# Kernel optimization log

Hardware: AMD Instinct MI355X
Metric: run time of the kernel (lower is better)

Reference implementation:

```python
import jax, jax.numpy as jnp
import numpy as np

N, E, D, R = 50000, 800000, 256, 16


def setup_inputs() -> dict:
    key = jax.random.key(0)
    ks = jax.random.split(key, 6)
    x = jax.random.normal(ks[0], (N, D), dtype=jnp.float32)
    edge_index = jax.random.randint(ks[1], (2, E), 0, N)
    edge_type = jax.random.randint(ks[2], (E,), 0, R)
    # FastRGCNConv params (num_bases=None): full relation weight, root weight, bias
    weight = jax.random.normal(ks[3], (R, D, 1), dtype=jnp.float32) / np.float32(np.sqrt(D))
    root = jax.random.normal(ks[4], (D, 1), dtype=jnp.float32) / np.float32(np.sqrt(D))
    bias = jnp.zeros((1,), dtype=jnp.float32)
    return dict(x=x, edge_index=edge_index, edge_type=edge_type,
                weight=weight, root=root, bias=bias)


def reference(x, edge_index, edge_type, weight, root, bias):
    n = x.shape[0]
    src, dst = edge_index[0], edge_index[1]  # messages flow src (j) -> dst (i)
    # per-edge relation-wise transform: (x_j @ W[r])  with out_channels == 1
    w_e = weight[edge_type, :, 0]                   # [E, D] gather of relation weights
    msg = jnp.sum(x[src] * w_e, axis=-1)            # [E] per-edge scalar message
    # mean aggregation over incoming edges (scatter-add / degree)
    agg = jax.ops.segment_sum(msg, dst, num_segments=n)                   # [N]
    cnt = jax.ops.segment_sum(jnp.ones_like(msg), dst, num_segments=n)    # [N]
    mean = agg / jnp.maximum(cnt, 1.0)
    # root transform + bias, then tanh nonlinearity (min_score is None)
    score = jnp.tanh(mean + (x @ root)[:, 0] + bias[0])                   # [N]
    x_out = x * score[:, None]
    return x_out, score
```

## Files before the change

### kernel.cpp

```cpp
#include <hip/hip_runtime.h>
#include <math.h>

#define D 256
#define NREL 16
#define CHUNK 6250
#define BPC 32
#define LDST 129

typedef float f4v __attribute__((ext_vector_type(4)));

__global__ __launch_bounds__(256) void rgcn_y_kernel(
    const float* __restrict__ x, const float* __restrict__ w,
    const float* __restrict__ root, float* __restrict__ y,
    float* __restrict__ xr, int n)
{
    __shared__ float lds[64 * LDST];
    const int t = threadIdx.x;
    const int nl = t & 63;
    const int rg = __builtin_amdgcn_readfirstlane(t >> 6);
    const int node = blockIdx.x * 64 + nl;
    const int base = blockIdx.x * 64;

    const float* w0 = w + (size_t)(rg * 4 + 0) * D;
    const float* w1 = w + (size_t)(rg * 4 + 1) * D;
    const float* w2 = w + (size_t)(rg * 4 + 2) * D;
    const float* w3 = w + (size_t)(rg * 4 + 3) * D;
    const float* w4 = (rg == 3) ? root : w0;

    float acc0 = 0.f, acc1 = 0.f, acc2 = 0.f, acc3 = 0.f, accR = 0.f;

    #pragma unroll
    for (int h = 0; h < 2; ++h) {
        #pragma unroll
        for (int k = 0; k < 8; ++k) {
            int flat = k * 256 + t;
            int snl  = flat >> 5;
            int f4i  = flat & 31;
            int gn   = base + snl;
            float4 v = make_float4(0.f, 0.f, 0.f, 0.f);
            if (gn < n)
                v = *reinterpret_cast<const float4*>(
                        x + (size_t)gn * D + h * 128 + f4i * 4);
            int a = snl * LDST + f4i * 4;
            lds[a + 0] = v.x; lds[a + 1] = v.y;
            lds[a + 2] = v.z; lds[a + 3] = v.w;
        }
        __syncthreads();

        const float* h0 = w0 + h * 128;
        const float* h1 = w1 + h * 128;
        const float* h2 = w2 + h * 128;
        const float* h3 = w3 + h * 128;
        const float* h4 = w4 + h * 128;
        #pragma unroll 16
        for (int d = 0; d < 128; ++d) {
            float xv = lds[nl * LDST + d];
            acc0 = fmaf(xv, h0[d], acc0);
            acc1 = fmaf(xv, h1[d], acc1);
            acc2 = fmaf(xv, h2[d], acc2);
            acc3 = fmaf(xv, h3[d], acc3);
            accR = fmaf(xv, h4[d], accR);
        }
        if (h == 0) __syncthreads();
    }

    if (node < n) {
        float4 o; o.x = acc0; o.y = acc1; o.z = acc2; o.w = acc3;
        *reinterpret_cast<float4*>(y + (size_t)node * NREL + rg * 4) = o;
        if (rg == 3) xr[node] = accR;
    }
}

__global__ __launch_bounds__(1024) void rgcn_edge_scan_kernel(
    const int* __restrict__ src, const int* __restrict__ dst,
    const int* __restrict__ et, const float* __restrict__ y,
    float2* __restrict__ partial, int e, int sl)
{
    __shared__ float lsum[CHUNK];
    __shared__ float lcnt[CHUNK];
    const int t = threadIdx.x;
    const int c = blockIdx.x / BPC;
    const int b = blockIdx.x % BPC;
    const int base = c * CHUNK;

    for (int j = t; j < CHUNK; j += 1024) { lsum[j] = 0.f; lcnt[j] = 0.f; }
    __syncthreads();

    const int slice0 = b * sl;
    const int rem = e - slice0;
    if (rem > 0) {
        const int gmax = (min(sl, rem) + 3) >> 2;
        for (int g = t; g < gmax; g += 1024) {
            int idx = slice0 + g * 4;
            if (idx + 3 < e) {
                int4 d4 = *reinterpret_cast<const int4*>(dst + idx);
                int4 s4 = *reinterpret_cast<const int4*>(src + idx);
                int4 r4 = *reinterpret_cast<const int4*>(et + idx);
                int loc0 = d4.x - base, loc1 = d4.y - base;
                int loc2 = d4.z - base, loc3 = d4.w - base;
                if ((unsigned)loc0 < (unsigned)CHUNK) {
                    atomicAdd(&lsum[loc0], y[(size_t)s4.x * NREL + r4.x]);
                    atomicAdd(&lcnt[loc0], 1.0f);
                }
                if ((unsigned)loc1 < (unsigned)CHUNK) {
                    atomicAdd(&lsum[loc1], y[(size_t)s4.y * NREL + r4.y]);
                    atomicAdd(&lcnt[loc1], 1.0f);
                }
                if ((unsigned)loc2 < (unsigned)CHUNK) {
                    atomicAdd(&lsum[loc2], y[(size_t)s4.z * NREL + r4.z]);
                    atomicAdd(&lcnt[loc2], 1.0f);
                }
                if ((unsigned)loc3 < (unsigned)CHUNK) {
                    atomicAdd(&lsum[loc3], y[(size_t)s4.w * NREL + r4.w]);
                    atomicAdd(&lcnt[loc3], 1.0f);
                }
            } else {
                for (int k = idx; k < e; ++k) {
                    int loc = dst[k] - base;
                    if ((unsigned)loc < (unsigned)CHUNK) {
                        atomicAdd(&lsum[loc], y[(size_t)src[k] * NREL + et[k]]);
                        atomicAdd(&lcnt[loc], 1.0f);
                    }
                }
            }
        }
    }
    __syncthreads();

    float2* p = partial + ((size_t)(c * BPC + b)) * CHUNK;
    for (int j = t; j < CHUNK; j += 1024)
        p[j] = make_float2(lsum[j], lcnt[j]);
}

__global__ __launch_bounds__(256) void rgcn_finish_kernel(
    const float2* __restrict__ partial, const float* __restrict__ xr,
    const float* __restrict__ bias, const float* __restrict__ x,
    float* __restrict__ out_x, float* __restrict__ out_score, int n)
{
    __shared__ float ssum[32], scnt[32], sc[32];
    const int t = threadIdx.x;
    const int base = blockIdx.x * 32;

    if (t < 32) { ssum[t] = 0.f; scnt[t] = 0.f; }
    __syncthreads();

    {
        int nl = t & 31;
        int bg = t >> 5;
        int node = base + nl;
        float s = 0.f, cN = 0.f;
        if (node < n) {
            int c = node / CHUNK;
            int j = node - c * CHUNK;
            const float2* p = partial + (size_t)c * BPC * CHUNK + j;
            #pragma unroll
            for (int b = 0; b < 4; ++b) {
                float2 v = p[(size_t)(bg * 4 + b) * CHUNK];
                s += v.x; cN += v.y;
            }
        }
        atomicAdd(&ssum[nl], s);
        atomicAdd(&scnt[nl], cN);
    }
    __syncthreads();

    if (t < 32) {
        int node = base + t;
        if (node < n) {
            float m = ssum[t] / fmaxf(scnt[t], 1.0f);
            float v = tanhf(m + xr[node] + bias[0]);
            sc[t] = v;
            out_score[node] = v;
        }
    }
    __syncthreads();

    #pragma unroll
    for (int k = 0; k < 8; ++k) {
        int nl = k * 4 + (t >> 6);
        int f4 = t & 63;
        int node = base + nl;
        if (node < n) {
            float s = sc[nl];
            float4 v = *reinterpret_cast<const float4*>(
                           x + (size_t)node * D + f4 * 4);
            v.x *= s; v.y *= s; v.z *= s; v.w *= s;
            f4v vo = {v.x, v.y, v.z, v.w};
            __builtin_nontemporal_store(
                vo, (f4v*)(out_x + (size_t)node * D + f4 * 4));
        }
    }
}

__global__ __launch_bounds__(256) void rgcn_reduce_score_kernel(
    const float2* __restrict__ partial, const float* __restrict__ xr,
    const float* __restrict__ bias, float* __restrict__ score, int n)
{
    int i = blockIdx.x * 256 + threadIdx.x;
    if (i < n) {
        int c = i / CHUNK;
        int j = i - c * CHUNK;
        const float2* p = partial + (size_t)c * BPC * CHUNK + j;
        float s = 0.f, cN = 0.f;
        #pragma unroll 8
        for (int b = 0; b < BPC; ++b) {
            float2 v = p[(size_t)b * CHUNK];
            s += v.x; cN += v.y;
        }
        float m = s / fmaxf(cN, 1.0f);
        score[i] = tanhf(m + xr[i] + bias[0]);
    }
}

__global__ __launch_bounds__(256) void rgcn_scale_kernel(
    const float* __restrict__ x, const float* __restrict__ score,
    float* __restrict__ xo, int n)
{
    int gid = blockIdx.x * 256 + threadIdx.x;
    int node = gid >> 6;
    int f4 = gid & 63;
    if (node < n) {
        float s = score[node];
        float4 v = *reinterpret_cast<const float4*>(
                       x + (size_t)node * D + f4 * 4);
        v.x *= s; v.y *= s; v.z *= s; v.w *= s;
        *reinterpret_cast<float4*>(xo + (size_t)node * D + f4 * 4) = v;
    }
}

extern "C" void kernel_launch(void* const* d_in, const int* in_sizes, int n_in,
                              void* d_out, int out_size, void* d_ws, size_t ws_size,
                              hipStream_t stream)
{
    const float* x    = (const float*)d_in[0];
    const int*   ei   = (const int*)d_in[1];
    const int*   et   = (const int*)d_in[2];
    const float* w    = (const float*)d_in[3];
    const float* root = (const float*)d_in[4];
    const float* bias = (const float*)d_in[5];

    const int n = in_sizes[0] / D;
    const int e = in_sizes[2];

    float* out       = (float*)d_out;
    float* out_x     = out;
    float* out_score = out + (size_t)n * D;

    const int C = (n + CHUNK - 1) / CHUNK;
    const int sl = ((((e + BPC - 1) / BPC) + 3) & ~3);

    const size_t part_f = (size_t)C * BPC * CHUNK * 2;
    const size_t need_f = part_f + (size_t)n * (NREL + 1);
    const bool use_ws = (ws_size >= need_f * sizeof(float));

    float* sb;
    if (use_ws)
        sb = (float*)d_ws;
    else {
        size_t ts = (((size_t)n * D - need_f) & ~(size_t)1);
        sb = out_x + ts;
    }
    float2* partial = (float2*)sb;
    float*  y  = sb + part_f;
    float*  xr = y + (size_t)n * NREL;

    dim3 blk(256);
    rgcn_y_kernel<<<dim3((n + 63) / 64), blk, 0, stream>>>(x, w, root, y, xr, n);

    rgcn_edge_scan_kernel<<<dim3(C * BPC), dim3(1024), 0, stream>>>(
        ei, ei + e, et, y, partial, e, sl);

    if (use_ws) {
        rgcn_finish_kernel<<<dim3((n + 31) / 32), blk, 0, stream>>>(
            partial, xr, bias, x, out_x, out_score, n);
    } else {
        rgcn_reduce_score_kernel<<<dim3((n + 255) / 256), blk, 0, stream>>>(
            partial, xr, bias, out_score, n);
        rgcn_scale_kernel<<<dim3((int)(((size_t)n * 64 + 255) / 256)), blk, 0, stream>>>(
            x, out_score, out_x, n);
    }
}
```

Measured before the change: 61.22 us.

## Rewrite node-relation projection to use direct coalesced loads and shuffle reduction

The projection kernel no longer stages x tiles through LDS with barriers. Each 16-lane group now reads two node rows straight from global memory with float4 loads, computes partial dot products against all 16 relation weights and the root vector, and reduces them with xor shuffles. It then writes one relation output per lane. This removes the LDS round trip and the syncthreads, but costs many more registers per thread (34 accumulators) and adds shuffle reduction work.

```diff
diff --git a/kernel.cpp b/kernel.cpp
--- a/kernel.cpp
+++ b/kernel.cpp
@@ -5,7 +5,6 @@
 #define NREL 16
 #define CHUNK 6250
 #define BPC 32
-#define LDST 129
 
 typedef float f4v __attribute__((ext_vector_type(4)));
 
@@ -14,60 +13,76 @@
     const float* __restrict__ root, float* __restrict__ y,
     float* __restrict__ xr, int n)
 {
-    __shared__ float lds[64 * LDST];
-    const int t = threadIdx.x;
-    const int nl = t & 63;
-    const int rg = __builtin_amdgcn_readfirstlane(t >> 6);
-    const int node = blockIdx.x * 64 + nl;
-    const int base = blockIdx.x * 64;
-
-    const float* w0 = w + (size_t)(rg * 4 + 0) * D;
-    const float* w1 = w + (size_t)(rg * 4 + 1) * D;
-    const float* w2 = w + (size_t)(rg * 4 + 2) * D;
-    const float* w3 = w + (size_t)(rg * 4 + 3) * D;
-    const float* w4 = (rg == 3) ? root : w0;
-
-    float acc0 = 0.f, acc1 = 0.f, acc2 = 0.f, acc3 = 0.f, accR = 0.f;
-
-    #pragma unroll
-    for (int h = 0; h < 2; ++h) {
+    const int t    = threadIdx.x;
+    const int lane = t & 63;
+    const int wv   = t >> 6;
+    const int grp  = lane >> 4;
+    const int s    = lane & 15;
+    const int node0 = blockIdx.x * 32 + wv * 8 + grp;
+    const int node1 = node0 + 4;
+
+    float accA[NREL + 1], accB[NREL + 1];
+    #pragma unroll
+    for (int r = 0; r <= NREL; ++r) { accA[r] = 0.f; accB[r] = 0.f; }
+
+    const bool okA = (node0 < n);
+    const bool okB = (node1 < n);
+    const float* xrowA = x + (size_t)node0 * D;
+    const float* xrowB = x + (size_t)node1 * D;
+
+    #pragma unroll
+    for (int k = 0; k < 4; ++k) {
+        const int off = k * 64 + s * 4;
+        float4 xa = make_float4(0.f, 0.f, 0.f, 0.f);
+        float4 xb = make_float4(0.f, 0.f, 0.f, 0.f);
+        if (okA) xa = *reinterpret_cast<const float4*>(xrowA + off);
+        if (okB) xb = *reinterpret_cast<const float4*>(xrowB + off);
         #pragma unroll
-        for (int k = 0; k < 8; ++k) {
-            int flat = k * 256 + t;
-            int snl  = flat >> 5;
-            int f4i  = flat & 31;
-            int gn   = base + snl;
-            float4 v = make_float4(0.f, 0.f, 0.f, 0.f);
-            if (gn < n)
-                v = *reinterpret_cast<const float4*>(
-                        x + (size_t)gn * D + h * 128 + f4i * 4);
-            int a = snl * LDST + f4i * 4;
-            lds[a + 0] = v.x; lds[a + 1] = v.y;
-            lds[a + 2] = v.z; lds[a + 3] = v.w;
-        }
-        __syncthreads();
-
-        const float* h0 = w0 + h * 128;
-        const float* h1 = w1 + h * 128;
-        const float* h2 = w2 + h * 128;
-        const float* h3 = w3 + h * 128;
-        const float* h4 = w4 + h * 128;
-        #pragma unroll 16
-        for (int d = 0; d < 128; ++d) {
-            float xv = lds[nl * LDST + d];
-            acc0 = fmaf(xv, h0[d], acc0);
-            acc1 = fmaf(xv, h1[d], acc1);
-            acc2 = fmaf(xv, h2[d], acc2);
-            acc3 = fmaf(xv, h3[d], acc3);
-            accR = fmaf(xv, h4[d], accR);
-        }
-        if (h == 0) __syncthreads();
-    }
-
-    if (node < n) {
-        float4 o; o.x = acc0; o.y = acc1; o.z = acc2; o.w = acc3;
-        *reinterpret_cast<float4*>(y + (size_t)node * NREL + rg * 4) = o;
-        if (rg == 3) xr[node] = accR;
+        for (int r = 0; r < NREL; ++r) {
+            float4 wv4 = *reinterpret_cast<const float4*>(
+                             w + (size_t)r * D + off);
+            accA[r] = fmaf(xa.x, wv4.x, accA[r]);
+            accA[r] = fmaf(xa.y, wv4.y, accA[r]);
+            accA[r] = fmaf(xa.z, wv4.z, accA[r]);
+            accA[r] = fmaf(xa.w, wv4.w, accA[r]);
+            accB[r] = fmaf(xb.x, wv4.x, accB[r]);
+            accB[r] = fmaf(xb.y, wv4.y, accB[r]);
+            accB[r] = fmaf(xb.z, wv4.z, accB[r]);
+            accB[r] = fmaf(xb.w, wv4.w, accB[r]);
+        }
+        float4 rv = *reinterpret_cast<const float4*>(root + off);
+        accA[NREL] = fmaf(xa.x, rv.x, accA[NREL]);
+        accA[NREL] = fmaf(xa.y, rv.y, accA[NREL]);
+        accA[NREL] = fmaf(xa.z, rv.z, accA[NREL]);
+        accA[NREL] = fmaf(xa.w, rv.w, accA[NREL]);
+        accB[NREL] = fmaf(xb.x, rv.x, accB[NREL]);
+        accB[NREL] = fmaf(xb.y, rv.y, accB[NREL]);
+        accB[NREL] = fmaf(xb.z, rv.z, accB[NREL]);
+        accB[NREL] = fmaf(xb.w, rv.w, accB[NREL]);
+    }
+
+    #pragma unroll
+    for (int r = 0; r <= NREL; ++r) {
+        #pragma unroll
+        for (int m = 8; m >= 1; m >>= 1) {
+            accA[r] += __shfl_xor(accA[r], m, 16);
+            accB[r] += __shfl_xor(accB[r], m, 16);
+        }
+    }
+
+    float ya = accA[0], yb = accB[0];
+    #pragma unroll
+    for (int r = 1; r < NREL; ++r) {
+        if (s == r) { ya = accA[r]; yb = accB[r]; }
+    }
+
+    if (okA) {
+        y[(size_t)node0 * NREL + s] = ya;
+        if (s == 0) xr[node0] = accA[NREL];
+    }
+    if (okB) {
+        y[(size_t)node1 * NREL + s] = yb;
+        if (s == 0) xr[node1] = accB[NREL];
     }
 }
 
@@ -265,7 +280,7 @@
     float*  xr = y + (size_t)n * NREL;
 
     dim3 blk(256);
-    rgcn_y_kernel<<<dim3((n + 63) / 64), blk, 0, stream>>>(x, w, root, y, xr, n);
+    rgcn_y_kernel<<<dim3((n + 31) / 32), blk, 0, stream>>>(x, w, root, y, xr, n);
 
     rgcn_edge_scan_kernel<<<dim3(C * BPC), dim3(1024), 0, stream>>>(
         ei, ei + e, et, y, partial, e, sl);
```

Result: slower. 64.52 us (+5.4%).

## Restructure y kernel to 512 threads with transposed swizzled LDS tile

Applied to the files above, without the earlier changes.

The per-node relation projection kernel now loads the whole 64x256 x tile into LDS in one pass, stored transposed with a rotation swizzle to avoid bank conflicts, instead of two padded half-tiles. Each block runs 8 waves that each compute 2 relations (the last wave also computes the root projection), replacing 4 waves of 4 relations. This doubles the waves available for latency hiding and halves the per-thread FMA chain, at the cost of 64 KB of LDS per block, which limits occupancy, and an uneven extra load on the last wave.

```diff
diff --git a/kernel.cpp b/kernel.cpp
--- a/kernel.cpp
+++ b/kernel.cpp
@@ -5,69 +5,72 @@
 #define NREL 16
 #define CHUNK 6250
 #define BPC 32
-#define LDST 129
 
 typedef float f4v __attribute__((ext_vector_type(4)));
 
-__global__ __launch_bounds__(256) void rgcn_y_kernel(
+__global__ __launch_bounds__(512) void rgcn_y_kernel(
     const float* __restrict__ x, const float* __restrict__ w,
     const float* __restrict__ root, float* __restrict__ y,
     float* __restrict__ xr, int n)
 {
-    __shared__ float lds[64 * LDST];
-    const int t = threadIdx.x;
-    const int nl = t & 63;
-    const int rg = __builtin_amdgcn_readfirstlane(t >> 6);
-    const int node = blockIdx.x * 64 + nl;
+    __shared__ float lds[D * 64];
+    const int t    = threadIdx.x;
+    const int nl   = t & 63;
+    const int rg   = __builtin_amdgcn_readfirstlane(t >> 6);
     const int base = blockIdx.x * 64;
-
-    const float* w0 = w + (size_t)(rg * 4 + 0) * D;
-    const float* w1 = w + (size_t)(rg * 4 + 1) * D;
-    const float* w2 = w + (size_t)(rg * 4 + 2) * D;
-    const float* w3 = w + (size_t)(rg * 4 + 3) * D;
-    const float* w4 = (rg == 3) ? root : w0;
-
-    float acc0 = 0.f, acc1 = 0.f, acc2 = 0.f, acc3 = 0.f, accR = 0.f;
-
+    const int node = base + nl;
+
+    const int f4i = t & 63;
     #pragma unroll
-    for (int h = 0; h < 2; ++h) {
-        #pragma unroll
-        for (int k = 0; k < 8; ++k) {
-            int flat = k * 256 + t;
-            int snl  = flat >> 5;
-            int f4i  = flat & 31;
-            int gn   = base + snl;
-            float4 v = make_float4(0.f, 0.f, 0.f, 0.f);
-            if (gn < n)
-                v = *reinterpret_cast<const float4*>(
-                        x + (size_t)gn * D + h * 128 + f4i * 4);
-            int a = snl * LDST + f4i * 4;
-            lds[a + 0] = v.x; lds[a + 1] = v.y;
-            lds[a + 2] = v.z; lds[a + 3] = v.w;
-        }
-        __syncthreads();
-
-        const float* h0 = w0 + h * 128;
-        const float* h1 = w1 + h * 128;
-        const float* h2 = w2 + h * 128;
-        const float* h3 = w3 + h * 128;
-        const float* h4 = w4 + h * 128;
-        #pragma unroll 16
-        for (int d = 0; d < 128; ++d) {
-            float xv = lds[nl * LDST + d];
-            acc0 = fmaf(xv, h0[d], acc0);
-            acc1 = fmaf(xv, h1[d], acc1);
-            acc2 = fmaf(xv, h2[d], acc2);
-            acc3 = fmaf(xv, h3[d], acc3);
-            accR = fmaf(xv, h4[d], accR);
-        }
-        if (h == 0) __syncthreads();
+    for (int k = 0; k < 8; ++k) {
+        int snl = k * 8 + (t >> 6);
+        int gn  = base + snl;
+        float4 v = make_float4(0.f, 0.f, 0.f, 0.f);
+        if (gn < n)
+            v = *reinterpret_cast<const float4*>(x + (size_t)gn * D + f4i * 4);
+        int rsw = (snl + f4i) & 63;
+        lds[(f4i * 4 + 0) * 64 + rsw] = v.x;
+        lds[(f4i * 4 + 1) * 64 + rsw] = v.y;
+        lds[(f4i * 4 + 2) * 64 + rsw] = v.z;
+        lds[(f4i * 4 + 3) * 64 + rsw] = v.w;
+    }
+    __syncthreads();
+
+    const float* w0 = w + (size_t)(rg * 2 + 0) * D;
+    const float* w1 = w + (size_t)(rg * 2 + 1) * D;
+
+    float a0 = 0.f, a1 = 0.f, aR = 0.f;
+    if (rg < 7) {
+        #pragma unroll 8
+        for (int q = 0; q < 64; ++q) {
+            int rs = (nl + q) & 63;
+            #pragma unroll
+            for (int j = 0; j < 4; ++j) {
+                int d = q * 4 + j;
+                float xv = lds[d * 64 + rs];
+                a0 = fmaf(xv, w0[d], a0);
+                a1 = fmaf(xv, w1[d], a1);
+            }
+        }
+    } else {
+        #pragma unroll 8
+        for (int q = 0; q < 64; ++q) {
+            int rs = (nl + q) & 63;
+            #pragma unroll
+            for (int j = 0; j < 4; ++j) {
+                int d = q * 4 + j;
+                float xv = lds[d * 64 + rs];
+                a0 = fmaf(xv, w0[d], a0);
+                a1 = fmaf(xv, w1[d], a1);
+                aR = fmaf(xv, root[d], aR);
+            }
+        }
     }
 
     if (node < n) {
-        float4 o; o.x = acc0; o.y = acc1; o.z = acc2; o.w = acc3;
-        *reinterpret_cast<float4*>(y + (size_t)node * NREL + rg * 4) = o;
-        if (rg == 3) xr[node] = accR;
+        float2 o; o.x = a0; o.y = a1;
+        *reinterpret_cast<float2*>(y + (size_t)node * NREL + rg * 2) = o;
+        if (rg == 7) xr[node] = aR;
     }
 }
 
@@ -264,19 +267,19 @@
     float*  y  = sb + part_f;
     float*  xr = y + (size_t)n * NREL;
 
-    dim3 blk(256);
-    rgcn_y_kernel<<<dim3((n + 63) / 64), blk, 0, stream>>>(x, w, root, y, xr, n);
+    rgcn_y_kernel<<<dim3((n + 63) / 64), dim3(512), 0, stream>>>(
+        x, w, root, y, xr, n);
 
     rgcn_edge_scan_kernel<<<dim3(C * BPC), dim3(1024), 0, stream>>>(
         ei, ei + e, et, y, partial, e, sl);
 
     if (use_ws) {
-        rgcn_finish_kernel<<<dim3((n + 31) / 32), blk, 0, stream>>>(
+        rgcn_finish_kernel<<<dim3((n + 31) / 32), dim3(256), 0, stream>>>(
             partial, xr, bias, x, out_x, out_score, n);
     } else {
-        rgcn_reduce_score_kernel<<<dim3((n + 255) / 256), blk, 0, stream>>>(
+        rgcn_reduce_score_kernel<<<dim3((n + 255) / 256), dim3(256), 0, stream>>>(
             partial, xr, bias, out_score, n);
-        rgcn_scale_kernel<<<dim3((int)(((size_t)n * 64 + 255) / 256)), blk, 0, stream>>>(
+        rgcn_scale_kernel<<<dim3((int)(((size_t)n * 64 + 255) / 256)), dim3(256), 0, stream>>>(
             x, out_score, out_x, n);
     }
 }
```

After: 67.01 us. +9.5%, slower.
